# Performance work log

Hardware: AMD Instinct MI355X
Metric: run time of the kernel (lower is better)

Reference implementation:

```python
import jax, jax.numpy as jnp
import numpy as np

N_NODES = 100000
N_EDGES = 1600000
NUM_GRAPHS = 128
F_IN = 64
HID = 64


def setup_inputs() -> dict:
    key = jax.random.key(0)
    ks = jax.random.split(key, 10)
    x = jax.random.normal(ks[0], (N_NODES, F_IN), dtype=jnp.float32)
    edge_index = jax.random.randint(ks[1], (2, N_EDGES), 0, N_NODES, dtype=jnp.int64)
    batch = jnp.sort(jax.random.randint(ks[2], (N_NODES,), 0, NUM_GRAPHS, dtype=jnp.int64))
    def glorot(k, shape):
        lim = float(np.sqrt(6.0 / (shape[0] + shape[1])))
        return jax.random.uniform(k, shape, dtype=jnp.float32, minval=-lim, maxval=lim)
    return {
        "x": x,
        "edge_index": edge_index,
        "batch": batch,
        "W1": glorot(ks[3], (F_IN, HID)), "b1": jnp.zeros((HID,), jnp.float32),
        "W2": glorot(ks[4], (HID, HID)), "b2": jnp.zeros((HID,), jnp.float32),
        "W3": glorot(ks[5], (HID, HID)), "b3": jnp.zeros((HID,), jnp.float32),
        "fc1_w": glorot(ks[6], (HID, 10)), "fc1_b": jnp.zeros((10,), jnp.float32),
        "fc2_w": glorot(ks[7], (10, 1)), "fc2_b": jnp.zeros((1,), jnp.float32),
    }


def reference(x, edge_index, batch, W1, b1, W2, b2, W3, b3, fc1_w, fc1_b, fc2_w, fc2_b):
    n = x.shape[0]
    # GCN normalization with self-loops (PyG gcn_norm): deg over dst incl. self-loop
    loop = jnp.arange(n, dtype=edge_index.dtype)
    src = jnp.concatenate([edge_index[0], loop])
    dst = jnp.concatenate([edge_index[1], loop])
    deg = jax.ops.segment_sum(jnp.ones_like(dst, dtype=x.dtype), dst, num_segments=n)
    dinv = jnp.where(deg > 0, jax.lax.rsqrt(deg), 0.0)
    norm = (dinv[src] * dinv[dst])[:, None]  # [E+N, 1]

    def gcn_conv(h, W, b):
        h = h @ W                      # dense linear transform
        msg = h[src] * norm            # gather + degree normalize
        agg = jax.ops.segment_sum(msg, dst, num_segments=n)  # scatter-add
        return agg + b

    h = jax.nn.relu(gcn_conv(x, W1, b1))
    h = jax.nn.relu(gcn_conv(h, W2, b2))
    h = jax.nn.relu(gcn_conv(h, W3, b3))

    # global mean pool over graphs
    sums = jax.ops.segment_sum(h, batch, num_segments=NUM_GRAPHS)
    counts = jax.ops.segment_sum(jnp.ones((n,), h.dtype), batch, num_segments=NUM_GRAPHS)
    pooled = sums / jnp.maximum(counts, 1.0)[:, None]  # [NUM_GRAPHS, HID]

    out = jax.nn.relu(pooled @ fc1_w + fc1_b)
    return out @ fc2_w + fc2_b  # [NUM_GRAPHS, 1]
```

## Files before the change

### kernel.cpp

```cpp
#include <hip/hip_runtime.h>
#include <hip/hip_fp16.h>

#define N_NODES   100000
#define N_EDGES   1600000
#define NUM_GRAPHS 128
#define HID       64

#define NB   512
#define NPB  196
#define NBU  511
#define CPE  3125
#define CSR_TOT (N_EDGES + N_NODES)


__global__ void k_zero(int* __restrict__ p, int n) {
  int i = blockIdx.x * blockDim.x + threadIdx.x;
  if (i < n) p[i] = 0;
}

__global__ void k_f2h(const float* __restrict__ in, __half* __restrict__ out, int n4) {
  int i = blockIdx.x * blockDim.x + threadIdx.x;
  if (i >= n4) return;
  float4 v = ((const float4*)in)[i];
  ((__half2*)out)[2 * i]     = __floats2half2_rn(v.x, v.y);
  ((__half2*)out)[2 * i + 1] = __floats2half2_rn(v.z, v.w);
}

__global__ __launch_bounds__(256) void k_b1a(const int* __restrict__ dst, int* __restrict__ H) {
  __shared__ int hist[NB];
  int w = blockIdx.x, t = threadIdx.x;
  for (int b = t; b < NB; b += 256) hist[b] = 0;
  __syncthreads();
  int e0 = w * CPE;
  for (int i = t; i < CPE; i += 256)
    atomicAdd(&hist[dst[e0 + i] / NPB], 1);
  __syncthreads();
  for (int b = t; b < NB; b += 256) H[w * NB + b] = hist[b];
}

__global__ __launch_bounds__(256) void k_colsum(const int* __restrict__ H, int* __restrict__ S) {
  __shared__ int red[256];
  int b = blockIdx.x, t = threadIdx.x;
  red[t] = H[t * NB + b] + H[(t + 256) * NB + b];
  __syncthreads();
  for (int d = 128; d > 0; d >>= 1) { if (t < d) red[t] += red[t + d]; __syncthreads(); }
  if (t == 0) S[b] = red[0];
}

__global__ __launch_bounds__(512) void k_rowscan(const int* __restrict__ H,
                                                 const int* __restrict__ S,
                                                 int* __restrict__ bstart,
                                                 int* __restrict__ OT) {
  __shared__ int sb[NB];
  __shared__ int sc[NB];
  int b = blockIdx.x, t = threadIdx.x;
  int sv = S[t];
  sb[t] = sv; __syncthreads();
  for (int d = 1; d < NB; d <<= 1) {
    int x = (t >= d) ? sb[t - d] : 0; __syncthreads();
    sb[t] += x; __syncthreads();
  }
  int bst = sb[b] - S[b];
  if (t == 0) bstart[b] = bst;
  if (b == NB - 1 && t == 0) bstart[NB] = sb[NB - 1];
  int v = H[t * NB + b];
  sc[t] = v; __syncthreads();
  for (int d = 1; d < NB; d <<= 1) {
    int x = (t >= d) ? sc[t - d] : 0; __syncthreads();
    sc[t] += x; __syncthreads();
  }
  OT[b * NB + t] = bst + sc[t] - v;
}

__global__ __launch_bounds__(256) void k_b1b(const int* __restrict__ src,
                                             const int* __restrict__ dst,
                                             const int* __restrict__ OT,
                                             int2* __restrict__ staged) {
  __shared__ int pos[NB];
  int w = blockIdx.x, t = threadIdx.x;
  for (int b = t; b < NB; b += 256) pos[b] = OT[b * NB + w];
  __syncthreads();
  int e0 = w * CPE;
  for (int i = t; i < CPE; i += 256) {
    int s = src[e0 + i], d = dst[e0 + i];
    int p = atomicAdd(&pos[d / NPB], 1);
    staged[p] = make_int2(s, d);
  }
}

__global__ __launch_bounds__(256) void k_b2a(const int2* __restrict__ staged,
                                             const int* __restrict__ bstart,
                                             int* __restrict__ row_off,
                                             float* __restrict__ dinv) {
  __shared__ int cnt[256];
  __shared__ int sc[256];
  int b = blockIdx.x, t = threadIdx.x;
  int nloc = min(NPB, N_NODES - b * NPB);
  cnt[t] = 0;
  __syncthreads();
  int s0 = bstart[b], s1 = bstart[b + 1];
  for (int i = s0 + t; i < s1; i += 256)
    atomicAdd(&cnt[staged[i].y - b * NPB], 1);
  __syncthreads();
  int v = (t < nloc) ? cnt[t] + 1 : 0;
  sc[t] = v; __syncthreads();
  for (int d = 1; d < 256; d <<= 1) {
    int x = (t >= d) ? sc[t - d] : 0; __syncthreads();
    sc[t] += x; __syncthreads();
  }
  if (t < nloc) {
    int g = b * NPB + t;
    row_off[g] = bstart[b] + b * NPB + (sc[t] - v);
    dinv[g] = rsqrtf((float)(cnt[t] + 1));
  }
  if (b == 0 && t == 0) row_off[N_NODES] = CSR_TOT;
}

__global__ __launch_bounds__(256) void k_b2b(const int2* __restrict__ staged,
                                             const int* __restrict__ bstart,
                                             const int* __restrict__ row_off,
                                             const float* __restrict__ dinv,
                                             int2* __restrict__ csr) {
  __shared__ int pos[NPB];
  __shared__ float dl[NPB];
  int b = blockIdx.x, t = threadIdx.x;
  int nloc = min(NPB, N_NODES - b * NPB);
  if (t < nloc) {
    int g = b * NPB + t;
    int ro = row_off[g];
    float dv = dinv[g];
    csr[ro] = make_int2(g, __float_as_int(dv * dv));
    pos[t] = ro + 1;
    dl[t] = dv;
  }
  __syncthreads();
  int s0 = bstart[b], s1 = bstart[b + 1];
  for (int i = s0 + t; i < s1; i += 256) {
    int2 e = staged[i];
    int l = e.y - b * NPB;
    int p = atomicAdd(&pos[l], 1);
    csr[p] = make_int2(e.x, __float_as_int(dl[l] * dinv[e.x]));
  }
}


__global__ __launch_bounds__(256) void k_dhist(const int* __restrict__ row_off,
                                               int* __restrict__ dbins) {
  __shared__ int h[256];
  int t = threadIdx.x;
  h[t] = 0;
  __syncthreads();
  int v = blockIdx.x * 256 + t;
  if (v < N_NODES) {
    int deg = min(row_off[v + 1] - row_off[v], 255);
    atomicAdd(&h[deg], 1);
  }
  __syncthreads();
  if (h[t] > 0) atomicAdd(&dbins[t], h[t]);
}

__global__ __launch_bounds__(256) void k_dscan(const int* __restrict__ dbins,
                                               int* __restrict__ dpos) {
  __shared__ int sc[256];
  int t = threadIdx.x;
  int v = dbins[t];
  sc[t] = v; __syncthreads();
  for (int d = 1; d < 256; d <<= 1) {
    int x = (t >= d) ? sc[t - d] : 0; __syncthreads();
    sc[t] += x; __syncthreads();
  }
  dpos[t] = sc[t] - v;
}

__global__ __launch_bounds__(256) void k_dperm(const int* __restrict__ row_off,
                                               int* __restrict__ dpos,
                                               int* __restrict__ perm) {
  __shared__ int cnt[256];
  __shared__ int sbase[256];
  int t = threadIdx.x;
  cnt[t] = 0;
  __syncthreads();
  int v = blockIdx.x * 256 + t;
  int bin = 0, rank = 0;
  if (v < N_NODES) {
    bin = min(row_off[v + 1] - row_off[v], 255);
    rank = atomicAdd(&cnt[bin], 1);
  }
  __syncthreads();
  if (cnt[t] > 0) sbase[t] = atomicAdd(&dpos[t], cnt[t]);
  __syncthreads();
  if (v < N_NODES) perm[sbase[bin] + rank] = v;
}


__global__ __launch_bounds__(256) void k_gemm(const __half* __restrict__ A,
                                              const float* __restrict__ W,
                                              __half* __restrict__ C) {
  __shared__ float sW[64 * 64];
  __shared__ float sA[64][65];
  int tid = threadIdx.x;
  #pragma unroll
  for (int i = tid; i < 1024; i += 256)
    ((float4*)sW)[i] = ((const float4*)W)[i];
  int row0 = blockIdx.x * 64;
  #pragma unroll
  for (int i = tid; i < 1024; i += 256) {
    int r = i >> 4, c4 = (i & 15) << 2;
    int row = row0 + r;
    if (row < N_NODES) {
      __half2 a = *(const __half2*)(A + (size_t)row * 64 + c4);
      __half2 b = *(const __half2*)(A + (size_t)row * 64 + c4 + 2);
      float2 fa = __half22float2(a), fb = __half22float2(b);
      sA[r][c4 + 0] = fa.x; sA[r][c4 + 1] = fa.y;
      sA[r][c4 + 2] = fb.x; sA[r][c4 + 3] = fb.y;
    } else {
      sA[r][c4 + 0] = 0.f; sA[r][c4 + 1] = 0.f; sA[r][c4 + 2] = 0.f; sA[r][c4 + 3] = 0.f;
    }
  }
  __syncthreads();
  int tr = (tid >> 4) << 2;
  int tc = (tid & 15) << 2;
  float acc[4][4];
  #pragma unroll
  for (int i = 0; i < 4; ++i)
    #pragma unroll
    for (int j = 0; j < 4; ++j) acc[i][j] = 0.f;
  #pragma unroll 8
  for (int k = 0; k < 64; ++k) {
    float4 w = *(const float4*)&sW[k * 64 + tc];
    float a0 = sA[tr + 0][k], a1 = sA[tr + 1][k], a2 = sA[tr + 2][k], a3 = sA[tr + 3][k];
    acc[0][0] += a0 * w.x; acc[0][1] += a0 * w.y; acc[0][2] += a0 * w.z; acc[0][3] += a0 * w.w;
    acc[1][0] += a1 * w.x; acc[1][1] += a1 * w.y; acc[1][2] += a1 * w.z; acc[1][3] += a1 * w.w;
    acc[2][0] += a2 * w.x; acc[2][1] += a2 * w.y; acc[2][2] += a2 * w.z; acc[2][3] += a2 * w.w;
    acc[3][0] += a3 * w.x; acc[3][1] += a3 * w.y; acc[3][2] += a3 * w.z; acc[3][3] += a3 * w.w;
  }
  #pragma unroll
  for (int i = 0; i < 4; ++i) {
    int row = row0 + tr + i;
    if (row < N_NODES) {
      *(__half2*)(C + (size_t)row * 64 + tc)     = __floats2half2_rn(acc[i][0], acc[i][1]);
      *(__half2*)(C + (size_t)row * 64 + tc + 2) = __floats2half2_rn(acc[i][2], acc[i][3]);
    }
  }
}


__device__ __forceinline__ void fma8(float* acc, float n, uint4 h) {
  __half2 u0 = *(__half2*)&h.x, u1 = *(__half2*)&h.y;
  __half2 u2 = *(__half2*)&h.z, u3 = *(__half2*)&h.w;
  float2 f0 = __half22float2(u0), f1 = __half22float2(u1);
  float2 f2 = __half22float2(u2), f3 = __half22float2(u3);
  acc[0] = fmaf(n, f0.x, acc[0]); acc[1] = fmaf(n, f0.y, acc[1]);
  acc[2] = fmaf(n, f1.x, acc[2]); acc[3] = fmaf(n, f1.y, acc[3]);
  acc[4] = fmaf(n, f2.x, acc[4]); acc[5] = fmaf(n, f2.y, acc[5]);
  acc[6] = fmaf(n, f3.x, acc[6]); acc[7] = fmaf(n, f3.y, acc[7]);
}

__global__ __launch_bounds__(256) void k_agg(const __half* __restrict__ hw,
                                             const int* __restrict__ row_off,
                                             const int2* __restrict__ csr,
                                             const int* __restrict__ perm,
                                             const float* __restrict__ bias,
                                             __half* __restrict__ out) {
  int tid = threadIdx.x;
  int lane = tid & 63;
  int sg = lane >> 3;
  int k = lane & 7;
  int slot = (blockIdx.x * 4 + (tid >> 6)) * 8 + sg;
  int v = -1, o = 0, d = 1;
  if (slot < N_NODES) {
    v = perm[slot];
    o = row_off[v];
    d = row_off[v + 1] - o;
  }
  int m = d;
  m = max(m, __shfl_xor(m, 8));
  m = max(m, __shfl_xor(m, 16));
  m = max(m, __shfl_xor(m, 32));
  float acc[8];
  #pragma unroll
  for (int j = 0; j < 8; ++j) acc[j] = 0.f;
  const __half* hk = hw + k * 8;
  int dm1 = d - 1;
  int i = 0;
  for (; i + 4 <= m; i += 4) {
    int2 p0 = csr[o + min(i + 0, dm1)];
    int2 p1 = csr[o + min(i + 1, dm1)];
    int2 p2 = csr[o + min(i + 2, dm1)];
    int2 p3 = csr[o + min(i + 3, dm1)];
    uint4 h0 = *(const uint4*)(hk + (size_t)p0.x * 64);
    uint4 h1 = *(const uint4*)(hk + (size_t)p1.x * 64);
    uint4 h2 = *(const uint4*)(hk + (size_t)p2.x * 64);
    uint4 h3 = *(const uint4*)(hk + (size_t)p3.x * 64);
    float n0 = (i + 0 < d) ? __int_as_float(p0.y) : 0.f;
    float n1 = (i + 1 < d) ? __int_as_float(p1.y) : 0.f;
    float n2 = (i + 2 < d) ? __int_as_float(p2.y) : 0.f;
    float n3 = (i + 3 < d) ? __int_as_float(p3.y) : 0.f;
    fma8(acc, n0, h0);
    fma8(acc, n1, h1);
    fma8(acc, n2, h2);
    fma8(acc, n3, h3);
  }
  for (; i < m; ++i) {
    int2 p = csr[o + min(i, dm1)];
    uint4 h = *(const uint4*)(hk + (size_t)p.x * 64);
    float n = (i < d) ? __int_as_float(p.y) : 0.f;
    fma8(acc, n, h);
  }
  if (v >= 0) {
    float4 b0 = *(const float4*)(bias + k * 8);
    float4 b1 = *(const float4*)(bias + k * 8 + 4);
    __half2 q0 = __floats2half2_rn(fmaxf(acc[0] + b0.x, 0.f), fmaxf(acc[1] + b0.y, 0.f));
    __half2 q1 = __floats2half2_rn(fmaxf(acc[2] + b0.z, 0.f), fmaxf(acc[3] + b0.w, 0.f));
    __half2 q2 = __floats2half2_rn(fmaxf(acc[4] + b1.x, 0.f), fmaxf(acc[5] + b1.y, 0.f));
    __half2 q3 = __floats2half2_rn(fmaxf(acc[6] + b1.z, 0.f), fmaxf(acc[7] + b1.w, 0.f));
    uint4 r;
    r.x = *(unsigned int*)&q0; r.y = *(unsigned int*)&q1;
    r.z = *(unsigned int*)&q2; r.w = *(unsigned int*)&q3;
    *(uint4*)(out + (size_t)v * HID + k * 8) = r;
  }
}


#define POOL_CHUNK 32

__global__ __launch_bounds__(256) void k_pool(const __half* __restrict__ h,
                                              const int* __restrict__ batch,
                                              float* __restrict__ pooled,
                                              int* __restrict__ pcnt) {
  int wid = threadIdx.x >> 6, lane = threadIdx.x & 63;
  int w = blockIdx.x * (blockDim.x >> 6) + wid;
  int v0 = w * POOL_CHUNK;
  if (v0 >= N_NODES) return;
  int vend = min(v0 + POOL_CHUNK, N_NODES);
  int g = batch[v0];
  float acc = 0.0f;
  int cnt = 0;
  for (int v = v0; v < vend; ++v) {
    int gv = batch[v];
    if (gv != g) {
      atomicAdd(&pooled[g * HID + lane], acc);
      if (lane == 0) atomicAdd(&pcnt[g], cnt);
      g = gv; acc = 0.0f; cnt = 0;
    }
    acc += __half2float(h[(size_t)v * HID + lane]);
    ++cnt;
  }
  atomicAdd(&pooled[g * HID + lane], acc);
  if (lane == 0) atomicAdd(&pcnt[g], cnt);
}

__global__ void k_mlp(const float* __restrict__ pooled, const int* __restrict__ pcnt,
                      const float* __restrict__ fc1w, const float* __restrict__ fc1b,
                      const float* __restrict__ fc2w, const float* __restrict__ fc2b,
                      float* __restrict__ out) {
  int g = threadIdx.x;
  if (g >= NUM_GRAPHS) return;
  float inv = 1.0f / fmaxf((float)pcnt[g], 1.0f);
  float hid[10];
  #pragma unroll
  for (int j = 0; j < 10; ++j) hid[j] = fc1b[j];
  for (int k = 0; k < HID; ++k) {
    float p = pooled[g * HID + k] * inv;
    #pragma unroll
    for (int j = 0; j < 10; ++j) hid[j] += p * fc1w[k * 10 + j];
  }
  float o = fc2b[0];
  #pragma unroll
  for (int j = 0; j < 10; ++j) o += fmaxf(hid[j], 0.0f) * fc2w[j];
  out[g] = o;
}


extern "C" void kernel_launch(void* const* d_in, const int* in_sizes, int n_in,
                              void* d_out, int out_size, void* d_ws, size_t ws_size,
                              hipStream_t stream) {
  const float* x    = (const float*)d_in[0];
  const int*   ei   = (const int*)d_in[1];
  const int*   batch= (const int*)d_in[2];
  const float* W1   = (const float*)d_in[3];
  const float* b1   = (const float*)d_in[4];
  const float* W2   = (const float*)d_in[5];
  const float* b2   = (const float*)d_in[6];
  const float* W3   = (const float*)d_in[7];
  const float* b3   = (const float*)d_in[8];
  const float* fc1w = (const float*)d_in[9];
  const float* fc1b = (const float*)d_in[10];
  const float* fc2w = (const float*)d_in[11];
  const float* fc2b = (const float*)d_in[12];

  const int* e_src = ei;
  const int* e_dst = ei + N_EDGES;

  char* ws = (char*)d_ws;
  auto alignup = [](size_t o, size_t a) { return (o + a - 1) / a * a; };
  size_t off = 0;
  int*   H      = (int*)(ws + off);  off += (size_t)NB * NB * 4;
  int*   pcnt   = (int*)(ws + off);  off += 128 * 4;
  float* pooled = (float*)(ws + off); off += 8192 * 4;
  int*   dbins  = (int*)(ws + off);  off += 256 * 4;
  const int ZERO_N = NB * NB + 128 + 8192 + 256;
  int*   S      = (int*)(ws + off);  off += NB * 4;
  int*   bstart = (int*)(ws + off);  off += (NB + 1) * 4;
  int*   dpos   = (int*)(ws + off);  off += 256 * 4;       off = alignup(off, 256);
  int*   OT     = (int*)(ws + off);  off += (size_t)NB * NB * 4;          off = alignup(off, 256);
  int*   row_off= (int*)(ws + off);  off += (size_t)(N_NODES + 1) * 4;    off = alignup(off, 256);
  float* dinv   = (float*)(ws + off); off += (size_t)N_NODES * 4;         off = alignup(off, 256);
  int*   perm   = (int*)(ws + off);  off += (size_t)N_NODES * 4;          off = alignup(off, 256);
  int2*  csr    = (int2*)(ws + off); off += (size_t)CSR_TOT * 8;          off = alignup(off, 256);
  __half* xh    = (__half*)(ws + off); off += (size_t)N_NODES * HID * 2;  off = alignup(off, 256);
  __half* h_a   = (__half*)(ws + off); off += (size_t)N_NODES * HID * 2;  off = alignup(off, 256);
  int2*  staged = (int2*)(ws + off);
  __half* h_b   = (__half*)(ws + off); off += (size_t)N_EDGES * 8;
  (void)ws_size; (void)in_sizes; (void)n_in; (void)out_size;

  const int TB = 256;
  const int NGRID = (N_NODES + TB - 1) / TB;
  k_zero   <<<(ZERO_N + TB - 1) / TB, TB, 0, stream>>>(H, ZERO_N);
  k_f2h    <<<(N_NODES * HID / 4 + TB - 1) / TB, TB, 0, stream>>>(x, xh, N_NODES * HID / 4);
  k_b1a    <<<NB, TB, 0, stream>>>(e_dst, H);
  k_colsum <<<NB, TB, 0, stream>>>(H, S);
  k_rowscan<<<NB, 512, 0, stream>>>(H, S, bstart, OT);
  k_b1b    <<<NB, TB, 0, stream>>>(e_src, e_dst, OT, staged);
  k_b2a    <<<NBU, TB, 0, stream>>>(staged, bstart, row_off, dinv);
  k_b2b    <<<NBU, TB, 0, stream>>>(staged, bstart, row_off, dinv, csr);
  k_dhist  <<<NGRID, TB, 0, stream>>>(row_off, dbins);
  k_dscan  <<<1, TB, 0, stream>>>(dbins, dpos);
  k_dperm  <<<NGRID, TB, 0, stream>>>(row_off, dpos, perm);

  const int GEMM_GRID = (N_NODES + 63) / 64;
  const int AGG_GRID  = (N_NODES + 31) / 32;

  k_gemm<<<GEMM_GRID, TB, 0, stream>>>(xh, W1, h_a);
  k_agg <<<AGG_GRID, TB, 0, stream>>>(h_a, row_off, csr, perm, b1, h_b);
  k_gemm<<<GEMM_GRID, TB, 0, stream>>>(h_b, W2, h_a);
  k_agg <<<AGG_GRID, TB, 0, stream>>>(h_a, row_off, csr, perm, b2, h_b);
  k_gemm<<<GEMM_GRID, TB, 0, stream>>>(h_b, W3, h_a);
  k_agg <<<AGG_GRID, TB, 0, stream>>>(h_a, row_off, csr, perm, b3, h_b);

  const int POOL_GRID = ((N_NODES + POOL_CHUNK - 1) / POOL_CHUNK + 3) / 4;
  k_pool<<<POOL_GRID, TB, 0, stream>>>(h_b, batch, pooled, pcnt);
  k_mlp <<<1, 128, 0, stream>>>(pooled, pcnt, fc1w, fc1b, fc2w, fc2b, (float*)d_out);
}
```

Measured before the change: 275.4 us.

## Fold zeroing and degree histogram into existing kernels, widen agg unroll with nontemporal CSR loads

Removes the k_zero and k_dhist launches. Zeroing of dbins moves into k_rowscan, pooled/pcnt zeroing moves into k_dscan, and the degree histogram is built in k_b2a with global atomics. The aggregation loop is unrolled from 4 to 8 edges, and CSR entries are read with nontemporal loads to raise memory-level parallelism and reduce cache pollution. In exchange it adds many global atomics on dbins, every rowscan block writes dbins redundantly, and there may be extra register pressure in k_agg.

After: 547.0 us. +98.6%, slower.

```diff
diff --git a/kernel.cpp b/kernel.cpp
--- a/kernel.cpp
+++ b/kernel.cpp
@@ -12,11 +12,6 @@
 #define CPE  3125
 #define CSR_TOT (N_EDGES + N_NODES)
 
-
-__global__ void k_zero(int* __restrict__ p, int n) {
-  int i = blockIdx.x * blockDim.x + threadIdx.x;
-  if (i < n) p[i] = 0;
-}
 
 __global__ void k_f2h(const float* __restrict__ in, __half* __restrict__ out, int n4) {
   int i = blockIdx.x * blockDim.x + threadIdx.x;
@@ -50,10 +45,12 @@
 __global__ __launch_bounds__(512) void k_rowscan(const int* __restrict__ H,
                                                  const int* __restrict__ S,
                                                  int* __restrict__ bstart,
-                                                 int* __restrict__ OT) {
+                                                 int* __restrict__ OT,
+                                                 int* __restrict__ dbins) {
   __shared__ int sb[NB];
   __shared__ int sc[NB];
   int b = blockIdx.x, t = threadIdx.x;
+  if (t < 256) dbins[t] = 0;
   int sv = S[t];
   sb[t] = sv; __syncthreads();
   for (int d = 1; d < NB; d <<= 1) {
@@ -91,7 +88,8 @@
 __global__ __launch_bounds__(256) void k_b2a(const int2* __restrict__ staged,
                                              const int* __restrict__ bstart,
                                              int* __restrict__ row_off,
-                                             float* __restrict__ dinv) {
+                                             float* __restrict__ dinv,
+                                             int* __restrict__ dbins) {
   __shared__ int cnt[256];
   __shared__ int sc[256];
   int b = blockIdx.x, t = threadIdx.x;
@@ -102,6 +100,7 @@
   for (int i = s0 + t; i < s1; i += 256)
     atomicAdd(&cnt[staged[i].y - b * NPB], 1);
   __syncthreads();
+  if (t < nloc) atomicAdd(&dbins[min(cnt[t] + 1, 255)], 1);
   int v = (t < nloc) ? cnt[t] + 1 : 0;
   sc[t] = v; __syncthreads();
   for (int d = 1; d < 256; d <<= 1) {
@@ -143,26 +142,15 @@
   }
 }
 
-
-__global__ __launch_bounds__(256) void k_dhist(const int* __restrict__ row_off,
-                                               int* __restrict__ dbins) {
-  __shared__ int h[256];
-  int t = threadIdx.x;
-  h[t] = 0;
-  __syncthreads();
-  int v = blockIdx.x * 256 + t;
-  if (v < N_NODES) {
-    int deg = min(row_off[v + 1] - row_off[v], 255);
-    atomicAdd(&h[deg], 1);
-  }
-  __syncthreads();
-  if (h[t] > 0) atomicAdd(&dbins[t], h[t]);
-}
-
 __global__ __launch_bounds__(256) void k_dscan(const int* __restrict__ dbins,
-                                               int* __restrict__ dpos) {
+                                               int* __restrict__ dpos,
+                                               float* __restrict__ pooled,
+                                               int* __restrict__ pcnt) {
   __shared__ int sc[256];
   int t = threadIdx.x;
+  #pragma unroll
+  for (int i = 0; i < 32; ++i) pooled[i * 256 + t] = 0.f;
+  if (t < 128) pcnt[t] = 0;
   int v = dbins[t];
   sc[t] = v; __syncthreads();
   for (int d = 1; d < 256; d <<= 1) {
@@ -254,6 +242,14 @@
   acc[2] = fmaf(n, f1.x, acc[2]); acc[3] = fmaf(n, f1.y, acc[3]);
   acc[4] = fmaf(n, f2.x, acc[4]); acc[5] = fmaf(n, f2.y, acc[5]);
   acc[6] = fmaf(n, f3.x, acc[6]); acc[7] = fmaf(n, f3.y, acc[7]);
+}
+
+__device__ __forceinline__ int2 nt_load_i2(const int2* p) {
+  unsigned long long raw = __builtin_nontemporal_load((const unsigned long long*)p);
+  int2 r;
+  r.x = (int)(unsigned int)(raw & 0xffffffffULL);
+  r.y = (int)(unsigned int)(raw >> 32);
+  return r;
 }
 
 __global__ __launch_bounds__(256) void k_agg(const __half* __restrict__ hw,
@@ -283,26 +279,21 @@
   const __half* hk = hw + k * 8;
   int dm1 = d - 1;
   int i = 0;
-  for (; i + 4 <= m; i += 4) {
-    int2 p0 = csr[o + min(i + 0, dm1)];
-    int2 p1 = csr[o + min(i + 1, dm1)];
-    int2 p2 = csr[o + min(i + 2, dm1)];
-    int2 p3 = csr[o + min(i + 3, dm1)];
-    uint4 h0 = *(const uint4*)(hk + (size_t)p0.x * 64);
-    uint4 h1 = *(const uint4*)(hk + (size_t)p1.x * 64);
-    uint4 h2 = *(const uint4*)(hk + (size_t)p2.x * 64);
-    uint4 h3 = *(const uint4*)(hk + (size_t)p3.x * 64);
-    float n0 = (i + 0 < d) ? __int_as_float(p0.y) : 0.f;
-    float n1 = (i + 1 < d) ? __int_as_float(p1.y) : 0.f;
-    float n2 = (i + 2 < d) ? __int_as_float(p2.y) : 0.f;
-    float n3 = (i + 3 < d) ? __int_as_float(p3.y) : 0.f;
-    fma8(acc, n0, h0);
-    fma8(acc, n1, h1);
-    fma8(acc, n2, h2);
-    fma8(acc, n3, h3);
+  for (; i + 8 <= m; i += 8) {
+    int2 p[8];
+    uint4 h[8];
+    #pragma unroll
+    for (int j = 0; j < 8; ++j) p[j] = nt_load_i2(csr + o + min(i + j, dm1));
+    #pragma unroll
+    for (int j = 0; j < 8; ++j) h[j] = *(const uint4*)(hk + (size_t)p[j].x * 64);
+    #pragma unroll
+    for (int j = 0; j < 8; ++j) {
+      float n = (i + j < d) ? __int_as_float(p[j].y) : 0.f;
+      fma8(acc, n, h[j]);
+    }
   }
   for (; i < m; ++i) {
-    int2 p = csr[o + min(i, dm1)];
+    int2 p = nt_load_i2(csr + o + min(i, dm1));
     uint4 h = *(const uint4*)(hk + (size_t)p.x * 64);
     float n = (i < d) ? __int_as_float(p.y) : 0.f;
     fma8(acc, n, h);
@@ -399,7 +390,6 @@
   int*   pcnt   = (int*)(ws + off);  off += 128 * 4;
   float* pooled = (float*)(ws + off); off += 8192 * 4;
   int*   dbins  = (int*)(ws + off);  off += 256 * 4;
-  const int ZERO_N = NB * NB + 128 + 8192 + 256;
   int*   S      = (int*)(ws + off);  off += NB * 4;
   int*   bstart = (int*)(ws + off);  off += (NB + 1) * 4;
   int*   dpos   = (int*)(ws + off);  off += 256 * 4;       off = alignup(off, 256);
@@ -416,16 +406,14 @@
 
   const int TB = 256;
   const int NGRID = (N_NODES + TB - 1) / TB;
-  k_zero   <<<(ZERO_N + TB - 1) / TB, TB, 0, stream>>>(H, ZERO_N);
   k_f2h    <<<(N_NODES * HID / 4 + TB - 1) / TB, TB, 0, stream>>>(x, xh, N_NODES * HID / 4);
   k_b1a    <<<NB, TB, 0, stream>>>(e_dst, H);
   k_colsum <<<NB, TB, 0, stream>>>(H, S);
-  k_rowscan<<<NB, 512, 0, stream>>>(H, S, bstart, OT);
+  k_rowscan<<<NB, 512, 0, stream>>>(H, S, bstart, OT, dbins);
   k_b1b    <<<NB, TB, 0, stream>>>(e_src, e_dst, OT, staged);
-  k_b2a    <<<NBU, TB, 0, stream>>>(staged, bstart, row_off, dinv);
+  k_b2a    <<<NBU, TB, 0, stream>>>(staged, bstart, row_off, dinv, dbins);
   k_b2b    <<<NBU, TB, 0, stream>>>(staged, bstart, row_off, dinv, csr);
-  k_dhist  <<<NGRID, TB, 0, stream>>>(row_off, dbins);
-  k_dscan  <<<1, TB, 0, stream>>>(dbins, dpos);
+  k_dscan  <<<1, TB, 0, stream>>>(dbins, dpos, pooled, pcnt);
   k_dperm  <<<NGRID, TB, 0, stream>>>(row_off, dpos, perm);
 
   const int GEMM_GRID = (N_NODES + 63) / 64;
```
